# Kernel optimization log

Measured on AMD Instinct MI355X. Metric: run time of the kernel, lower is better.

The kernel has to match this reference:

```python
import jax, jax.numpy as jnp
import numpy as np

N = 50000        # nodes
E = 800000       # edges (avg degree 16)
IN = 256         # in_size
H = 4            # heads
C = 32           # out_size per head
NEG_SLOPE = 0.2  # PyG GATConv leaky_relu slope
LN_EPS = 1e-5


def setup_inputs() -> dict:
    key = jax.random.key(0)
    ks = jax.random.split(key, 6)
    x = jax.random.normal(ks[0], (N, IN), dtype=jnp.float32)
    edge_index = jax.random.randint(ks[1], (2, E), 0, N, dtype=jnp.int32)
    W = jax.random.normal(ks[2], (IN, H * C), dtype=jnp.float32) * 0.05
    att_src = jax.random.normal(ks[3], (H, C), dtype=jnp.float32) * 0.05
    att_dst = jax.random.normal(ks[4], (H, C), dtype=jnp.float32) * 0.05
    bias = jnp.zeros((H * C,), dtype=jnp.float32)
    ln_gamma = jnp.ones((H * C,), dtype=jnp.float32)
    ln_beta = jnp.zeros((H * C,), dtype=jnp.float32)
    return {"x": x, "edge_index": edge_index, "W": W, "att_src": att_src,
            "att_dst": att_dst, "bias": bias, "ln_gamma": ln_gamma,
            "ln_beta": ln_beta}


def _segment_softmax(alpha, seg, num_segments):
    # alpha: [E, H], softmax over edges sharing the same destination node.
    amax = jax.ops.segment_max(alpha, seg, num_segments=num_segments)  # [N, H]
    amax = jnp.where(jnp.isfinite(amax), amax, 0.0)  # nodes with no in-edges
    ex = jnp.exp(alpha - amax[seg])
    denom = jax.ops.segment_sum(ex, seg, num_segments=num_segments)    # [N, H]
    return ex / (denom[seg] + 1e-16)


def reference(x, edge_index, W, att_src, att_dst, bias, ln_gamma, ln_beta):
    # --- GATConv (concat=True) ---
    x_lin = (x @ W).reshape(N, H, C)                    # [N, H, C]
    a_src = jnp.sum(x_lin * att_src, axis=-1)           # [N, H]
    a_dst = jnp.sum(x_lin * att_dst, axis=-1)           # [N, H]
    src, dst = edge_index[0], edge_index[1]             # messages src -> dst
    alpha = a_src[src] + a_dst[dst]                     # [E, H]
    alpha = jnp.where(alpha >= 0, alpha, NEG_SLOPE * alpha)
    alpha = _segment_softmax(alpha, dst, N)             # [E, H]
    msg = x_lin[src] * alpha[..., None]                 # [E, H, C]
    out = jax.ops.segment_sum(msg, dst, num_segments=N) # [N, H, C]
    out = out.reshape(N, H * C) + bias                  # [N, H*C]
    # --- LayerNorm over feature dim ---
    mu = jnp.mean(out, axis=-1, keepdims=True)
    var = jnp.mean(jnp.square(out - mu), axis=-1, keepdims=True)
    out = (out - mu) * jax.lax.rsqrt(var + LN_EPS) * ln_gamma + ln_beta
    # --- activation ---
    return jax.nn.relu(out)
```

## Files before the change

### kernel.cpp

```cpp
#include <hip/hip_runtime.h>

#define NNODES 50000
#define NEDGES 800000
#define INFEAT 256
#define HC 128
#define NH 4
#define CPH 32
#define XS 136

typedef unsigned int uint32;
typedef unsigned short u16;
typedef short short8 __attribute__((ext_vector_type(8)));
typedef float f32x4 __attribute__((ext_vector_type(4)));

__device__ __forceinline__ float b2f(u16 s) {
    uint32 u = ((uint32)s) << 16;
    return __builtin_bit_cast(float, u);
}
__device__ __forceinline__ u16 f2bf(float x) {
    uint32 u = __builtin_bit_cast(uint32, x);
    uint32 r = (u + 0x7FFFu + ((u >> 16) & 1u)) >> 16;
    return (u16)r;
}
__device__ __forceinline__ bool probe_bf16(const void* gamma) {
    return ((const uint32*)gamma)[0] == 0x3F803F80u;
}

__global__ __launch_bounds__(256) void wtp_kernel(const void* __restrict__ W,
                                                  const void* __restrict__ gm,
                                                  u16* __restrict__ wtp,
                                                  int* __restrict__ count) {
    const bool isbf = probe_bf16(gm);
    int c = blockIdx.x * 256 + threadIdx.x;
    int kt = c >> 9, nt = (c >> 6) & 7, l = c & 63;
    int r = l & 15, quad = l >> 4;
    int n = nt * 16 + r;
    int kbase = kt * 32 + quad * 8;
    u16 vals[8];
#pragma unroll
    for (int j = 0; j < 8; ++j) {
        int k = kbase + j;
        vals[j] = isbf ? ((const u16*)W)[k * HC + n] : f2bf(((const float*)W)[k * HC + n]);
    }
    *(uint4*)(wtp + (size_t)c * 8) = *(const uint4*)vals;
    for (int i = c; i < NNODES; i += 4096) count[i] = 0;
}

__global__ __launch_bounds__(256) void gemm_mfma(const void* __restrict__ x,
                                                 const uint4* __restrict__ wtp,
                                                 const void* __restrict__ att_src,
                                                 const void* __restrict__ att_dst,
                                                 const void* __restrict__ gm,
                                                 u16* __restrict__ xlinx,
                                                 float* __restrict__ adst) {
    const bool isbf = probe_bf16(gm);
    const int tid = threadIdx.x;
    int wave = blockIdx.x * 4 + (tid >> 6);
    int lane = tid & 63;
    int r = lane & 15;
    int quad = lane >> 4;
    int m0 = wave * 16;
    int arow = m0 + r;
    if (arow > NNODES - 1) arow = NNODES - 1;
    const size_t abase = (size_t)arow * INFEAT + quad * 8;

    f32x4 acc[8];
#pragma unroll
    for (int nt = 0; nt < 8; ++nt) acc[nt] = (f32x4){0.f, 0.f, 0.f, 0.f};

#pragma unroll
    for (int kt = 0; kt < 8; ++kt) {
        const int k0 = kt * 32;
        short8 afrag;
        if (isbf) {
            uint4 q = *(const uint4*)((const u16*)x + abase + k0);
            afrag = __builtin_bit_cast(short8, q);
        } else {
            const float* xp = (const float*)x + abase + k0;
            float4 f0 = *(const float4*)xp;
            float4 f1 = *(const float4*)(xp + 4);
            uint4 q;
            q.x = (uint32)f2bf(f0.x) | ((uint32)f2bf(f0.y) << 16);
            q.y = (uint32)f2bf(f0.z) | ((uint32)f2bf(f0.w) << 16);
            q.z = (uint32)f2bf(f1.x) | ((uint32)f2bf(f1.y) << 16);
            q.w = (uint32)f2bf(f1.z) | ((uint32)f2bf(f1.w) << 16);
            afrag = __builtin_bit_cast(short8, q);
        }
#pragma unroll
        for (int nt = 0; nt < 8; ++nt) {
            short8 bfrag = __builtin_bit_cast(short8, wtp[(kt * 8 + nt) * 64 + lane]);
            acc[nt] = __builtin_amdgcn_mfma_f32_16x16x32_bf16(afrag, bfrag, acc[nt], 0, 0, 0);
        }
    }
#pragma unroll
    for (int nt = 0; nt < 8; ++nt) {
#pragma unroll
        for (int reg = 0; reg < 4; ++reg) {
            int grow = m0 + quad * 4 + reg;
            if (grow < NNODES) xlinx[(size_t)grow * XS + nt * 16 + r] = f2bf(acc[nt][reg]);
        }
    }

    float asv[8], adv[8];
#pragma unroll
    for (int nt = 0; nt < 8; ++nt) {
        int c = nt * 16 + r;
        if (isbf) {
            asv[nt] = b2f(((const u16*)att_src)[c]);
            adv[nt] = b2f(((const u16*)att_dst)[c]);
        } else {
            asv[nt] = ((const float*)att_src)[c];
            adv[nt] = ((const float*)att_dst)[c];
        }
    }
    float psrc[4][4], pdst[4][4];
#pragma unroll
    for (int h = 0; h < 4; ++h)
#pragma unroll
        for (int reg = 0; reg < 4; ++reg) { psrc[h][reg] = 0.f; pdst[h][reg] = 0.f; }
#pragma unroll
    for (int nt = 0; nt < 8; ++nt) {
        const int h = nt >> 1;
#pragma unroll
        for (int reg = 0; reg < 4; ++reg) {
            psrc[h][reg] = fmaf(acc[nt][reg], asv[nt], psrc[h][reg]);
            pdst[h][reg] = fmaf(acc[nt][reg], adv[nt], pdst[h][reg]);
        }
    }
#pragma unroll
    for (int m = 1; m < 16; m <<= 1) {
#pragma unroll
        for (int h = 0; h < 4; ++h)
#pragma unroll
            for (int reg = 0; reg < 4; ++reg) {
                psrc[h][reg] += __shfl_xor(psrc[h][reg], m);
                pdst[h][reg] += __shfl_xor(pdst[h][reg], m);
            }
    }
#pragma unroll
    for (int reg = 0; reg < 4; ++reg)
#pragma unroll
        for (int h = 0; h < 4; ++h)
            if (r == reg * 4 + h) {
                int grow = m0 + quad * 4 + reg;
                if (grow < NNODES) {
                    *(float*)(xlinx + (size_t)grow * XS + 128 + h * 2) = psrc[h][reg];
                    adst[grow * 4 + h] = pdst[h][reg];
                }
            }
}

__global__ __launch_bounds__(256) void hist_kernel(const int* __restrict__ ei,
                                                   int* __restrict__ count,
                                                   int* __restrict__ rank) {
    int e = blockIdx.x * 256 + threadIdx.x;
    if (e < NEDGES) rank[e] = atomicAdd(&count[ei[NEDGES + e]], 1);
}

__global__ __launch_bounds__(256) void blkred_kernel(const int* __restrict__ count,
                                                     int* __restrict__ blksum) {
    int i = blockIdx.x * 256 + threadIdx.x;
    int v = (i < NNODES) ? count[i] : 0;
#pragma unroll
    for (int m = 1; m < 64; m <<= 1) v += __shfl_xor(v, m);
    __shared__ int s[4];
    if ((threadIdx.x & 63) == 0) s[threadIdx.x >> 6] = v;
    __syncthreads();
    if (threadIdx.x == 0) blksum[blockIdx.x] = s[0] + s[1] + s[2] + s[3];
}

__global__ __launch_bounds__(256) void scanout_kernel(const int* __restrict__ count,
                                                      const int* __restrict__ blksum,
                                                      int* __restrict__ offsets) {
    __shared__ int sb[256];
    __shared__ int sd[256];
    const int nblk = (NNODES + 255) / 256;
    int t = threadIdx.x;
    int bv = (t < nblk) ? blksum[t] : 0;
    sb[t] = bv;
    __syncthreads();
    for (int off = 1; off < 256; off <<= 1) {
        int tv = (t >= off) ? sb[t - off] : 0;
        __syncthreads();
        sb[t] += tv;
        __syncthreads();
    }
    int base = sb[blockIdx.x] - blksum[blockIdx.x];

    int i = blockIdx.x * 256 + t;
    int v = (i < NNODES) ? count[i] : 0;
    sd[t] = v;
    __syncthreads();
    for (int off = 1; off < 256; off <<= 1) {
        int tv = (t >= off) ? sd[t - off] : 0;
        __syncthreads();
        sd[t] += tv;
        __syncthreads();
    }
    if (i < NNODES) offsets[i] = base + sd[t] - v;
    if (i == 0) offsets[NNODES] = NEDGES;
}

__global__ __launch_bounds__(256) void scatter_kernel(const int* __restrict__ ei,
                                                      const int* __restrict__ offsets,
                                                      const int* __restrict__ rank,
                                                      int* __restrict__ col) {
    int e = blockIdx.x * 256 + threadIdx.x;
    if (e >= NEDGES) return;
    int d = ei[NEDGES + e];
    col[offsets[d] + rank[e]] = ei[e];
}

__global__ __launch_bounds__(256) void node_kernel(const u16* __restrict__ xlinx,
                                                   const float* __restrict__ adst,
                                                   const int* __restrict__ offsets,
                                                   const int* __restrict__ col,
                                                   const void* __restrict__ bias,
                                                   const void* __restrict__ gamma,
                                                   const void* __restrict__ beta,
                                                   void* __restrict__ out) {
    const bool isbf = probe_bf16(gamma);
    int node = blockIdx.x * 4 + (threadIdx.x >> 6);
    int lane = threadIdx.x & 63;
    int h = lane >> 4;
    int f2 = lane * 2;
    float adh = adst[node * 4 + h];
    int start = offsets[node];
    int end = offsets[node + 1];

    float dsum = 0.f, acc0 = 0.f, acc1 = 0.f;
    int i = start;
    for (; i + 7 < end; i += 8) {
        size_t bb[8];
        uint32 pf[8];
        float aw[8];
#pragma unroll
        for (int j = 0; j < 8; ++j) bb[j] = (size_t)col[i + j] * XS;
#pragma unroll
        for (int j = 0; j < 8; ++j) {
            pf[j] = *(const uint32*)(xlinx + bb[j] + f2);
            aw[j] = *(const float*)(xlinx + bb[j] + 128 + h * 2);
        }
#pragma unroll
        for (int j = 0; j < 8; ++j) {
            float a = aw[j] + adh;
            a = (a >= 0.f) ? a : 0.2f * a;
            float w = __expf(a);
            dsum += w;
            float x0 = __builtin_bit_cast(float, pf[j] << 16);
            float x1 = __builtin_bit_cast(float, pf[j] & 0xffff0000u);
            acc0 = fmaf(x0, w, acc0);
            acc1 = fmaf(x1, w, acc1);
        }
    }
    for (; i < end; ++i) {
        size_t bb = (size_t)col[i] * XS;
        uint32 p = *(const uint32*)(xlinx + bb + f2);
        float a = *(const float*)(xlinx + bb + 128 + h * 2) + adh;
        a = (a >= 0.f) ? a : 0.2f * a;
        float w = __expf(a);
        dsum += w;
        float x0 = __builtin_bit_cast(float, p << 16);
        float x1 = __builtin_bit_cast(float, p & 0xffff0000u);
        acc0 = fmaf(x0, w, acc0);
        acc1 = fmaf(x1, w, acc1);
    }
    float rden = 1.f / (dsum + 1e-16f);

    float bi0, bi1, g0, g1, be0, be1;
    if (isbf) {
        uint32 bb = ((const uint32*)bias)[lane];
        uint32 gg = ((const uint32*)gamma)[lane];
        uint32 eb = ((const uint32*)beta)[lane];
        bi0 = b2f((u16)(bb & 0xffffu)); bi1 = b2f((u16)(bb >> 16));
        g0  = b2f((u16)(gg & 0xffffu)); g1  = b2f((u16)(gg >> 16));
        be0 = b2f((u16)(eb & 0xffffu)); be1 = b2f((u16)(eb >> 16));
    } else {
        float2 tb = ((const float2*)bias)[lane];
        float2 tg = ((const float2*)gamma)[lane];
        float2 te = ((const float2*)beta)[lane];
        bi0 = tb.x; bi1 = tb.y; g0 = tg.x; g1 = tg.y; be0 = te.x; be1 = te.y;
    }
    float v0 = fmaf(acc0, rden, bi0);
    float v1 = fmaf(acc1, rden, bi1);
    float s2 = v0 + v1;
    float q2 = v0 * v0 + v1 * v1;
#pragma unroll
    for (int m = 1; m < 64; m <<= 1) {
        s2 += __shfl_xor(s2, m);
        q2 += __shfl_xor(q2, m);
    }
    float mean = s2 * (1.f / 128.f);
    float var = q2 * (1.f / 128.f) - mean * mean;
    float inv = rsqrtf(var + 1e-5f);
    float d0 = v0 - mean, d1 = v1 - mean;
    float o0 = fmaxf(fmaf(d0 * inv, g0, be0), 0.f);
    float o1 = fmaxf(fmaf(d1 * inv, g1, be1), 0.f);
    if (isbf) {
        uint32 po = (uint32)f2bf(o0) | ((uint32)f2bf(o1) << 16);
        ((uint32*)out)[(size_t)node * 64 + lane] = po;
    } else {
        float2 po; po.x = o0; po.y = o1;
        ((float2*)out)[(size_t)node * 64 + lane] = po;
    }
}

extern "C" void kernel_launch(void* const* d_in, const int* in_sizes, int n_in,
                              void* d_out, int out_size, void* d_ws, size_t ws_size,
                              hipStream_t stream) {
    const void* x       = d_in[0];
    const int*  ei      = (const int*)d_in[1];
    const void* W       = d_in[2];
    const void* att_src = d_in[3];
    const void* att_dst = d_in[4];
    const void* bias    = d_in[5];
    const void* gamma   = d_in[6];
    const void* beta    = d_in[7];

    char* w = (char*)d_ws;
    size_t off = 0;
    u16* xlinx   = (u16*)(w + off);   off += 13600000;
    u16* wtp     = (u16*)(w + off);   off += 65536;
    float* adst  = (float*)(w + off); off += 800000;
    int* count   = (int*)(w + off);   off += 200000;
    int* offsets = (int*)(w + off);   off += 200016;
    int* rank    = (int*)(w + off);   off += 3200000;
    int* blksum  = (int*)(w + off);   off += 1024;
    int* col     = (int*)(w + off);   off += 3200000;

    const int NBLK = (NNODES + 255) / 256;
    wtp_kernel<<<16, 256, 0, stream>>>(W, gamma, wtp, count);
    gemm_mfma<<<(NNODES + 63) / 64, 256, 0, stream>>>(x, (const uint4*)wtp, att_src, att_dst,
                                                      gamma, xlinx, adst);
    hist_kernel<<<(NEDGES + 255) / 256, 256, 0, stream>>>(ei, count, rank);
    blkred_kernel<<<NBLK, 256, 0, stream>>>(count, blksum);
    scanout_kernel<<<NBLK, 256, 0, stream>>>(count, blksum, offsets);
    scatter_kernel<<<(NEDGES + 255) / 256, 256, 0, stream>>>(ei, offsets, rank, col);
    node_kernel<<<NNODES / 4, 256, 0, stream>>>(xlinx, adst, offsets, col,
                                                bias, gamma, beta, d_out);
}
```

Baseline: 228.5 us.

## Stage GEMM A tile in LDS, split asrc from xlin, branchless gather tail

The GEMM now loads each wave's 16x256 input tile into shared memory with coalesced row-contiguous loads, converting to bf16 once, then reads MFMA A fragments from LDS. The packed 136-stride xlin row with embedded source attention scores is split into a dense 128-stride xlin plus a separate asrc array. The node kernel's remainder loop is folded into the 8-wide loop with clamped indices and zeroed weights. The aims are better global coalescing in the GEMM and less per-edge gather traffic. In exchange, asrc becomes a separate gather from another cache line, and the GEMM uses about 33 KB of LDS per block.

Measured after the change: 223.5 us. -2.2%, faster.

```diff
diff --git a/kernel.cpp b/kernel.cpp
--- a/kernel.cpp
+++ b/kernel.cpp
@@ -6,7 +6,7 @@
 #define HC 128
 #define NH 4
 #define CPH 32
-#define XS 136
+#define LSTRIDE 264
 
 typedef unsigned int uint32;
 typedef unsigned short u16;
@@ -51,18 +51,45 @@
                                                  const void* __restrict__ att_src,
                                                  const void* __restrict__ att_dst,
                                                  const void* __restrict__ gm,
-                                                 u16* __restrict__ xlinx,
+                                                 u16* __restrict__ xlin,
+                                                 float* __restrict__ asrc,
                                                  float* __restrict__ adst) {
+    __shared__ u16 atile[4 * 16 * LSTRIDE];
     const bool isbf = probe_bf16(gm);
     const int tid = threadIdx.x;
-    int wave = blockIdx.x * 4 + (tid >> 6);
-    int lane = tid & 63;
+    const int wv = tid >> 6;
+    const int lane = tid & 63;
+    int wave = blockIdx.x * 4 + wv;
     int r = lane & 15;
     int quad = lane >> 4;
     int m0 = wave * 16;
-    int arow = m0 + r;
-    if (arow > NNODES - 1) arow = NNODES - 1;
-    const size_t abase = (size_t)arow * INFEAT + quad * 8;
+    u16* my = atile + wv * (16 * LSTRIDE);
+
+    if (isbf) {
+#pragma unroll
+        for (int rep = 0; rep < 8; ++rep) {
+            int idx = rep * 64 + lane;
+            int row = idx >> 5;
+            int ch  = idx & 31;
+            int gr = m0 + row;
+            if (gr > NNODES - 1) gr = NNODES - 1;
+            uint4 q = *(const uint4*)((const u16*)x + (size_t)gr * INFEAT + ch * 8);
+            *(uint4*)(my + row * LSTRIDE + ch * 8) = q;
+        }
+    } else {
+#pragma unroll
+        for (int rep = 0; rep < 16; ++rep) {
+            int idx = rep * 64 + lane;
+            int row = idx >> 6;
+            int c4  = idx & 63;
+            int gr = m0 + row;
+            if (gr > NNODES - 1) gr = NNODES - 1;
+            float4 f = *(const float4*)((const float*)x + (size_t)gr * INFEAT + c4 * 4);
+            u16 v[4] = {f2bf(f.x), f2bf(f.y), f2bf(f.z), f2bf(f.w)};
+            *(uint2*)(my + row * LSTRIDE + c4 * 4) = *(const uint2*)v;
+        }
+    }
+    __syncthreads();
 
     f32x4 acc[8];
 #pragma unroll
@@ -70,22 +97,8 @@
 
 #pragma unroll
     for (int kt = 0; kt < 8; ++kt) {
-        const int k0 = kt * 32;
-        short8 afrag;
-        if (isbf) {
-            uint4 q = *(const uint4*)((const u16*)x + abase + k0);
-            afrag = __builtin_bit_cast(short8, q);
-        } else {
-            const float* xp = (const float*)x + abase + k0;
-            float4 f0 = *(const float4*)xp;
-            float4 f1 = *(const float4*)(xp + 4);
-            uint4 q;
-            q.x = (uint32)f2bf(f0.x) | ((uint32)f2bf(f0.y) << 16);
-            q.y = (uint32)f2bf(f0.z) | ((uint32)f2bf(f0.w) << 16);
-            q.z = (uint32)f2bf(f1.x) | ((uint32)f2bf(f1.y) << 16);
-            q.w = (uint32)f2bf(f1.z) | ((uint32)f2bf(f1.w) << 16);
-            afrag = __builtin_bit_cast(short8, q);
-        }
+        short8 afrag = __builtin_bit_cast(short8,
+            *(const uint4*)(my + r * LSTRIDE + kt * 32 + quad * 8));
 #pragma unroll
         for (int nt = 0; nt < 8; ++nt) {
             short8 bfrag = __builtin_bit_cast(short8, wtp[(kt * 8 + nt) * 64 + lane]);
@@ -97,7 +110,7 @@
 #pragma unroll
         for (int reg = 0; reg < 4; ++reg) {
             int grow = m0 + quad * 4 + reg;
-            if (grow < NNODES) xlinx[(size_t)grow * XS + nt * 16 + r] = f2bf(acc[nt][reg]);
+            if (grow < NNODES) xlin[(size_t)grow * HC + nt * 16 + r] = f2bf(acc[nt][reg]);
         }
     }
 
@@ -144,7 +157,7 @@
             if (r == reg * 4 + h) {
                 int grow = m0 + quad * 4 + reg;
                 if (grow < NNODES) {
-                    *(float*)(xlinx + (size_t)grow * XS + 128 + h * 2) = psrc[h][reg];
+                    asrc[grow * 4 + h] = psrc[h][reg];
                     adst[grow * 4 + h] = pdst[h][reg];
                 }
             }
@@ -211,7 +224,8 @@
     col[offsets[d] + rank[e]] = ei[e];
 }
 
-__global__ __launch_bounds__(256) void node_kernel(const u16* __restrict__ xlinx,
+__global__ __launch_bounds__(256) void node_kernel(const u16* __restrict__ xlin,
+                                                   const float* __restrict__ asrc,
                                                    const float* __restrict__ adst,
                                                    const int* __restrict__ offsets,
                                                    const int* __restrict__ col,
@@ -229,41 +243,31 @@
     int end = offsets[node + 1];
 
     float dsum = 0.f, acc0 = 0.f, acc1 = 0.f;
-    int i = start;
-    for (; i + 7 < end; i += 8) {
-        size_t bb[8];
+    for (int i = start; i < end; i += 8) {
+        int cc[8];
         uint32 pf[8];
         float aw[8];
 #pragma unroll
-        for (int j = 0; j < 8; ++j) bb[j] = (size_t)col[i + j] * XS;
-#pragma unroll
         for (int j = 0; j < 8; ++j) {
-            pf[j] = *(const uint32*)(xlinx + bb[j] + f2);
-            aw[j] = *(const float*)(xlinx + bb[j] + 128 + h * 2);
+            int idx = i + j;
+            cc[j] = col[idx < end ? idx : (end - 1)];
+        }
+#pragma unroll
+        for (int j = 0; j < 8; ++j) {
+            pf[j] = *(const uint32*)(xlin + (size_t)cc[j] * HC + f2);
+            aw[j] = asrc[cc[j] * 4 + h];
         }
 #pragma unroll
         for (int j = 0; j < 8; ++j) {
             float a = aw[j] + adh;
             a = (a >= 0.f) ? a : 0.2f * a;
-            float w = __expf(a);
+            float w = (i + j < end) ? __expf(a) : 0.f;
             dsum += w;
             float x0 = __builtin_bit_cast(float, pf[j] << 16);
             float x1 = __builtin_bit_cast(float, pf[j] & 0xffff0000u);
             acc0 = fmaf(x0, w, acc0);
             acc1 = fmaf(x1, w, acc1);
         }
-    }
-    for (; i < end; ++i) {
-        size_t bb = (size_t)col[i] * XS;
-        uint32 p = *(const uint32*)(xlinx + bb + f2);
-        float a = *(const float*)(xlinx + bb + 128 + h * 2) + adh;
-        a = (a >= 0.f) ? a : 0.2f * a;
-        float w = __expf(a);
-        dsum += w;
-        float x0 = __builtin_bit_cast(float, p << 16);
-        float x1 = __builtin_bit_cast(float, p & 0xffff0000u);
-        acc0 = fmaf(x0, w, acc0);
-        acc1 = fmaf(x1, w, acc1);
     }
     float rden = 1.f / (dsum + 1e-16f);
 
@@ -319,8 +323,9 @@
 
     char* w = (char*)d_ws;
     size_t off = 0;
-    u16* xlinx   = (u16*)(w + off);   off += 13600000;
+    u16* xlin    = (u16*)(w + off);   off += 12800000;
     u16* wtp     = (u16*)(w + off);   off += 65536;
+    float* asrc  = (float*)(w + off); off += 800000;
     float* adst  = (float*)(w + off); off += 800000;
     int* count   = (int*)(w + off);   off += 200000;
     int* offsets = (int*)(w + off);   off += 200016;
@@ -331,11 +336,11 @@
     const int NBLK = (NNODES + 255) / 256;
     wtp_kernel<<<16, 256, 0, stream>>>(W, gamma, wtp, count);
     gemm_mfma<<<(NNODES + 63) / 64, 256, 0, stream>>>(x, (const uint4*)wtp, att_src, att_dst,
-                                                      gamma, xlinx, adst);
+                                                      gamma, xlin, asrc, adst);
     hist_kernel<<<(NEDGES + 255) / 256, 256, 0, stream>>>(ei, count, rank);
     blkred_kernel<<<NBLK, 256, 0, stream>>>(count, blksum);
     scanout_kernel<<<NBLK, 256, 0, stream>>>(count, blksum, offsets);
     scatter_kernel<<<(NEDGES + 255) / 256, 256, 0, stream>>>(ei, offsets, rank, col);
-    node_kernel<<<NNODES / 4, 256, 0, stream>>>(xlinx, adst, offsets, col,
+    node_kernel<<<NNODES / 4, 256, 0, stream>>>(xlin, asrc, adst, offsets, col,
                                                 bias, gamma, beta, d_out);
 }
```
